# Performance work log

Measured on AMD Instinct MI355X. Metric: run time of the kernel, lower is better.

The kernel has to match this reference:

```python
import jax, jax.numpy as jnp
import numpy as np

D_K = 1  # global d_k from the source module


def setup_inputs() -> dict:
    key = jax.random.key(0)
    kq, kk, kv = jax.random.split(key, 3)
    B, H, S, Dv = 8, 8, 16384, 64
    Q = jax.random.normal(kq, (B, H, S, 1), dtype=jnp.float32)
    K = jax.random.normal(kk, (B, H, S, 1), dtype=jnp.float32)
    V = jax.random.normal(kv, (B, H, S, Dv), dtype=jnp.float32)
    return {"Q": Q, "K": K, "V": V}


def reference(Q, K, V):
    # Frobenius norm over the sequence axis (dim=2), unsqueezed at dim 3
    # K, Q: [B, H, S, 1] -> norm: [B, H, 1] -> [B, H, 1, 1]
    Kn = jnp.expand_dims(jnp.sqrt(jnp.sum(K * K, axis=2)), axis=3)
    Qn = jnp.expand_dims(jnp.sqrt(jnp.sum(Q * Q, axis=2)), axis=3)
    K = K / Kn
    Q = Q / Qn
    # Linear-attention reorder: (K^T V) first -> [B, H, 1, Dv]
    K_TV = jnp.einsum("bhsd,bhse->bhde", K, V) / np.float32(np.sqrt(D_K))
    # Q @ (K^T V) -> [B, H, S, Dv]
    context = jnp.einsum("bhsd,bhde->bhse", Q, K_TV)
    return context
```

## Files before the change

kernel.cpp:

```cpp
#include <hip/hip_runtime.h>
#include <math.h>

#define S_LEN 16384
#define DV    64
#define NBH   64
#define NBLK  16
#define CHUNK (S_LEN / NBLK)

typedef float vf4 __attribute__((ext_vector_type(4)));


__global__ __launch_bounds__(256) void stage1_partial(
    const float* __restrict__ Q, const float* __restrict__ K,
    const float* __restrict__ V,
    float* __restrict__ pktv, float* __restrict__ pqk) {
    const int bh  = blockIdx.x >> 4;
    const int blk = blockIdx.x & 15;
    const int tid = threadIdx.x;
    const int e4  = tid & 15;
    const int sg  = tid >> 4;

    const float* Kb = K + (size_t)bh * S_LEN + blk * CHUNK;
    const float* Qb = Q + (size_t)bh * S_LEN + blk * CHUNK;
    const vf4*   Vb = (const vf4*)(V + (size_t)bh * S_LEN * DV)
                      + (size_t)blk * CHUNK * (DV / 4);

    vf4 acc = {0.f, 0.f, 0.f, 0.f};
    #pragma unroll 4
    for (int i = 0; i < CHUNK / 16; ++i) {
        const int s = i * 16 + sg;
        const float k = Kb[s];
        const vf4 v = __builtin_nontemporal_load(Vb + s * (DV / 4) + e4);
        acc += k * v;
    }

    const vf4 q4 = ((const vf4*)Qb)[tid];
    const vf4 k4 = ((const vf4*)Kb)[tid];
    float qss = q4.x * q4.x + q4.y * q4.y + q4.z * q4.z + q4.w * q4.w;
    float kss = k4.x * k4.x + k4.y * k4.y + k4.z * k4.z + k4.w * k4.w;
    #pragma unroll
    for (int off = 32; off > 0; off >>= 1) {
        qss += __shfl_down(qss, off);
        kss += __shfl_down(kss, off);
    }

    __shared__ vf4 red[16][16];
    __shared__ float rq[4], rk[4];
    red[sg][e4] = acc;
    if ((tid & 63) == 0) { rq[tid >> 6] = qss; rk[tid >> 6] = kss; }
    __syncthreads();

    if (tid < DV) {
        const float* base = (const float*)red;
        float s = 0.f;
        #pragma unroll
        for (int p = 0; p < 16; ++p) s += base[p * DV + tid];
        pktv[((size_t)bh * NBLK + blk) * DV + tid] = s;
    }
    if (tid == 0) {
        pqk[(bh * NBLK + blk) * 2 + 0] = rq[0] + rq[1] + rq[2] + rq[3];
        pqk[(bh * NBLK + blk) * 2 + 1] = rk[0] + rk[1] + rk[2] + rk[3];
    }
}

__global__ __launch_bounds__(64) void stage2_finalize(
    const float* __restrict__ pktv, const float* __restrict__ pqk,
    float* __restrict__ fk) {
    const int bh  = blockIdx.x;
    const int tid = threadIdx.x;

    float qss = 0.f, kss = 0.f;
    if (tid < NBLK) {
        qss = pqk[(bh * NBLK + tid) * 2 + 0];
        kss = pqk[(bh * NBLK + tid) * 2 + 1];
    }
    #pragma unroll
    for (int off = 8; off > 0; off >>= 1) {
        qss += __shfl_down(qss, off);
        kss += __shfl_down(kss, off);
    }
    const float inv = 1.0f / (sqrtf(__shfl(qss, 0)) * sqrtf(__shfl(kss, 0)));

    float s = 0.f;
    #pragma unroll
    for (int p = 0; p < NBLK; ++p)
        s += pktv[((size_t)bh * NBLK + p) * DV + tid];
    fk[bh * DV + tid] = s * inv;
}

#define S3_BLOCKS 2048
#define F4_TOTAL  (NBH * S_LEN * (DV / 4))
#define F4_PER_BLOCK (F4_TOTAL / S3_BLOCKS)

__global__ __launch_bounds__(256) void stage3_outer(
    const float* __restrict__ Q, const float* __restrict__ fk,
    vf4* __restrict__ out) {
    const size_t base = (size_t)blockIdx.x * F4_PER_BLOCK;
    const int tid = threadIdx.x;
    const int bh  = (int)(base >> 18);
    const int e4  = tid & 15;
    const vf4 f = ((const vf4*)fk)[bh * 16 + e4];
    const float* Qb = Q + (size_t)bh * S_LEN;
    const int s0 = (int)((base >> 4) & (S_LEN - 1)) + (tid >> 4);

    #pragma unroll 8
    for (int t = 0; t < 32; ++t) {
        const float q = Qb[s0 + t * 16];
        __builtin_nontemporal_store(q * f, out + base + t * 256 + tid);
    }
}

extern "C" void kernel_launch(void* const* d_in, const int* in_sizes, int n_in,
                              void* d_out, int out_size, void* d_ws, size_t ws_size,
                              hipStream_t stream) {
    const float* Q = (const float*)d_in[0];
    const float* K = (const float*)d_in[1];
    const float* V = (const float*)d_in[2];
    float* out = (float*)d_out;

    float* pktv = (float*)d_ws;
    float* pqk  = pktv + (size_t)NBH * NBLK * DV;
    float* fk   = pqk + NBH * NBLK * 2;

    stage1_partial<<<NBH * NBLK, 256, 0, stream>>>(Q, K, V, pktv, pqk);
    stage2_finalize<<<NBH, 64, 0, stream>>>(pktv, pqk, fk);
    stage3_outer<<<S3_BLOCKS, 256, 0, stream>>>(Q, fk, (vf4*)out);
}
```

Measured before the change: 436.0 us.

## Fuse three stages into one cooperative kernel with grid-wide sync

Merges the partial K^T V reduction, the norm finalization and the outer-product write into a single cooperative kernel of 1024 blocks separated by a grid sync. Each block recomputes its bh's finalized vector into shared memory rather than reading it from a separate finalize kernel. This removes two kernel launches and their inter-kernel gaps. In exchange, all 1024 blocks must be co-resident, and a grid barrier is added.

```diff
diff --git a/kernel.cpp b/kernel.cpp
--- a/kernel.cpp
+++ b/kernel.cpp
@@ -1,33 +1,39 @@
 #include <hip/hip_runtime.h>
+#include <hip/hip_cooperative_groups.h>
 #include <math.h>
 
-#define S_LEN 16384
-#define DV    64
-#define NBH   64
-#define NBLK  16
-#define CHUNK (S_LEN / NBLK)
+#define S_LEN   16384
+#define DV      64
+#define NBH     64
+#define NBLOCKS 1024
+#define SUBS    (NBLOCKS / NBH)
+#define ROWS    (S_LEN / SUBS)
 
 typedef float vf4 __attribute__((ext_vector_type(4)));
+namespace cg = cooperative_groups;
 
-
-__global__ __launch_bounds__(256) void stage1_partial(
+__global__ __launch_bounds__(256, 4) void fused_all(
     const float* __restrict__ Q, const float* __restrict__ K,
     const float* __restrict__ V,
-    float* __restrict__ pktv, float* __restrict__ pqk) {
-    const int bh  = blockIdx.x >> 4;
-    const int blk = blockIdx.x & 15;
+    float* __restrict__ pktv,
+    float* __restrict__ pqk,
+    vf4* __restrict__ out) {
+
+    const int blk = blockIdx.x;
+    const int bh  = blk >> 4;
+    const int sub = blk & 15;
     const int tid = threadIdx.x;
     const int e4  = tid & 15;
     const int sg  = tid >> 4;
 
-    const float* Kb = K + (size_t)bh * S_LEN + blk * CHUNK;
-    const float* Qb = Q + (size_t)bh * S_LEN + blk * CHUNK;
+    const float* Kb = K + (size_t)bh * S_LEN + sub * ROWS;
+    const float* Qb = Q + (size_t)bh * S_LEN + sub * ROWS;
     const vf4*   Vb = (const vf4*)(V + (size_t)bh * S_LEN * DV)
-                      + (size_t)blk * CHUNK * (DV / 4);
+                      + (size_t)sub * ROWS * (DV / 4);
 
     vf4 acc = {0.f, 0.f, 0.f, 0.f};
     #pragma unroll 4
-    for (int i = 0; i < CHUNK / 16; ++i) {
+    for (int i = 0; i < ROWS / 16; ++i) {
         const int s = i * 16 + sg;
         const float k = Kb[s];
         const vf4 v = __builtin_nontemporal_load(Vb + s * (DV / 4) + e4);
@@ -36,8 +42,8 @@
 
     const vf4 q4 = ((const vf4*)Qb)[tid];
     const vf4 k4 = ((const vf4*)Kb)[tid];
-    float qss = q4.x * q4.x + q4.y * q4.y + q4.z * q4.z + q4.w * q4.w;
-    float kss = k4.x * k4.x + k4.y * k4.y + k4.z * k4.z + k4.w * k4.w;
+    float qss = q4.x*q4.x + q4.y*q4.y + q4.z*q4.z + q4.w*q4.w;
+    float kss = k4.x*k4.x + k4.y*k4.y + k4.z*k4.z + k4.w*k4.w;
     #pragma unroll
     for (int off = 32; off > 0; off >>= 1) {
         qss += __shfl_down(qss, off);
@@ -55,58 +61,38 @@
         float s = 0.f;
         #pragma unroll
         for (int p = 0; p < 16; ++p) s += base[p * DV + tid];
-        pktv[((size_t)bh * NBLK + blk) * DV + tid] = s;
+        pktv[(size_t)blk * DV + tid] = s;
     }
     if (tid == 0) {
-        pqk[(bh * NBLK + blk) * 2 + 0] = rq[0] + rq[1] + rq[2] + rq[3];
-        pqk[(bh * NBLK + blk) * 2 + 1] = rk[0] + rk[1] + rk[2] + rk[3];
+        pqk[blk * 2 + 0] = rq[0] + rq[1] + rq[2] + rq[3];
+        pqk[blk * 2 + 1] = rk[0] + rk[1] + rk[2] + rk[3];
     }
-}
 
-__global__ __launch_bounds__(64) void stage2_finalize(
-    const float* __restrict__ pktv, const float* __restrict__ pqk,
-    float* __restrict__ fk) {
-    const int bh  = blockIdx.x;
-    const int tid = threadIdx.x;
+    __threadfence();
+    cg::this_grid().sync();
 
-    float qss = 0.f, kss = 0.f;
-    if (tid < NBLK) {
-        qss = pqk[(bh * NBLK + tid) * 2 + 0];
-        kss = pqk[(bh * NBLK + tid) * 2 + 1];
+    __shared__ float fkl[DV];
+    if (tid < DV) {
+        float a = 0.f;
+        if (tid < 16)      a = pqk[(bh * 16 + tid) * 2 + 0];
+        else if (tid < 32) a = pqk[(bh * 16 + (tid - 16)) * 2 + 1];
+        #pragma unroll
+        for (int off = 8; off > 0; off >>= 1) a += __shfl_down(a, off);
+        const float inv = 1.0f / (sqrtf(__shfl(a, 0)) * sqrtf(__shfl(a, 16)));
+        float s = 0.f;
+        #pragma unroll
+        for (int p = 0; p < 16; ++p)
+            s += pktv[(size_t)(bh * 16 + p) * DV + tid];
+        fkl[tid] = s * inv;
     }
-    #pragma unroll
-    for (int off = 8; off > 0; off >>= 1) {
-        qss += __shfl_down(qss, off);
-        kss += __shfl_down(kss, off);
-    }
-    const float inv = 1.0f / (sqrtf(__shfl(qss, 0)) * sqrtf(__shfl(kss, 0)));
+    __syncthreads();
 
-    float s = 0.f;
-    #pragma unroll
-    for (int p = 0; p < NBLK; ++p)
-        s += pktv[((size_t)bh * NBLK + p) * DV + tid];
-    fk[bh * DV + tid] = s * inv;
-}
-
-#define S3_BLOCKS 2048
-#define F4_TOTAL  (NBH * S_LEN * (DV / 4))
-#define F4_PER_BLOCK (F4_TOTAL / S3_BLOCKS)
-
-__global__ __launch_bounds__(256) void stage3_outer(
-    const float* __restrict__ Q, const float* __restrict__ fk,
-    vf4* __restrict__ out) {
-    const size_t base = (size_t)blockIdx.x * F4_PER_BLOCK;
-    const int tid = threadIdx.x;
-    const int bh  = (int)(base >> 18);
-    const int e4  = tid & 15;
-    const vf4 f = ((const vf4*)fk)[bh * 16 + e4];
-    const float* Qb = Q + (size_t)bh * S_LEN;
-    const int s0 = (int)((base >> 4) & (S_LEN - 1)) + (tid >> 4);
-
+    const vf4 f = ((const vf4*)fkl)[e4];
+    vf4* ob = out + ((size_t)bh * S_LEN + (size_t)sub * ROWS) * (DV / 4);
     #pragma unroll 8
-    for (int t = 0; t < 32; ++t) {
-        const float q = Qb[s0 + t * 16];
-        __builtin_nontemporal_store(q * f, out + base + t * 256 + tid);
+    for (int t = 0; t < ROWS * (DV / 4) / 256; ++t) {
+        const float q = Qb[(tid >> 4) + t * 16];
+        __builtin_nontemporal_store(q * f, ob + t * 256 + tid);
     }
 }
 
@@ -116,13 +102,13 @@
     const float* Q = (const float*)d_in[0];
     const float* K = (const float*)d_in[1];
     const float* V = (const float*)d_in[2];
-    float* out = (float*)d_out;
 
     float* pktv = (float*)d_ws;
-    float* pqk  = pktv + (size_t)NBH * NBLK * DV;
-    float* fk   = pqk + NBH * NBLK * 2;
+    float* pqk  = pktv + (size_t)NBLOCKS * DV;
+    vf4*   out4 = (vf4*)d_out;
 
-    stage1_partial<<<NBH * NBLK, 256, 0, stream>>>(Q, K, V, pktv, pqk);
-    stage2_finalize<<<NBH, 64, 0, stream>>>(pktv, pqk, fk);
-    stage3_outer<<<S3_BLOCKS, 256, 0, stream>>>(Q, fk, (vf4*)out);
+    void* args[] = {(void*)&Q, (void*)&K, (void*)&V,
+                    (void*)&pktv, (void*)&pqk, (void*)&out4};
+    hipLaunchCooperativeKernel((const void*)fused_all, dim3(NBLOCKS), dim3(256),
+                               args, 0, stream);
 }
```

New measurement: 680.1 us. +56.0%, slower.
